# Performance work log

Hardware: AMD Instinct MI355X
Metric: run time of the kernel (lower is better)

Reference implementation:

```python
import jax, jax.numpy as jnp
import numpy as np

TAU = 0.07          # temperature
TOP_N_SIM = 5       # n_neighb for KNN label assignment
RANKING_K = 4       # top-k same/diff-class sims for confidence ratio


def setup_inputs() -> dict:
    key = jax.random.key(0)
    k1, k2, k3 = jax.random.split(key, 3)
    n_src, n_tgt, d, n_cls = 8192, 6144, 256, 64
    return {
        "source_features": jax.random.normal(k1, (n_src, d), dtype=jnp.float32),
        "source_labels": jax.random.randint(k2, (n_src,), 0, n_cls, dtype=jnp.int32),
        "target_features": jax.random.normal(k3, (n_tgt, d), dtype=jnp.float32),
    }


def _l2_normalize(x):
    # F.normalize(x, dim=1, p=2) with eps=1e-12
    n = jnp.sqrt(jnp.sum(x * x, axis=1, keepdims=True))
    return x / jnp.maximum(n, 1e-12)


def reference(source_features, source_labels, target_features):
    n_tgt = target_features.shape[0]
    top_ranked_n = n_tgt * 2 // 3

    # cosine similarity matrix [n_src, n_tgt]
    sim = _l2_normalize(source_features) @ _l2_normalize(target_features).T

    # sort each column descending over sources
    order = jnp.argsort(-sim, axis=0)                      # [S, T]

    # KNN label assignment with torch.mode semantics (tie -> smallest value)
    neigh = source_labels[order[:TOP_N_SIM]]               # [K, T]
    counts = (neigh[:, None, :] == neigh[None, :, :]).sum(axis=1)  # [K, T]
    maxc = counts.max(axis=0)                              # [T]
    big = jnp.iinfo(source_labels.dtype).max
    assigned = jnp.where(counts == maxc[None, :], neigh, big).min(axis=0)  # [T]

    # sims & labels reordered by descending similarity, per column
    sorted_sims = jnp.take_along_axis(sim, order, axis=0)  # [S, T]
    sorted_labels = source_labels[order]                   # [S, T]
    pos = sorted_labels == assigned[None, :]               # [S, T]

    def first_k_masked_sum(mask):
        # sum of first RANKING_K sorted sims where mask is True, per column
        csum = jnp.cumsum(mask.astype(sim.dtype), axis=0)
        sel = mask & (csum <= RANKING_K)
        return jnp.sum(jnp.where(sel, sorted_sims, 0.0), axis=0)

    nln = first_k_masked_sum(pos)
    nun = first_k_masked_sum(~pos)
    scores = jax.lax.stop_gradient(nln / nun)              # [T], detached

    _, top_ind = jax.lax.top_k(scores, top_ranked_n)       # confident targets
    conf_sim = sim[:, top_ind]                             # [S, top_ranked_n]
    conf_lab = assigned[top_ind]

    # contrastive softmax loss over sources
    mask_sim = (source_labels[:, None] == conf_lab[None, :]).astype(sim.dtype)
    exp_scores = jax.nn.softmax(conf_sim / TAU, axis=0)
    contrastive = (exp_scores * mask_sim).sum(axis=0) / exp_scores.sum(axis=0)
    return -jnp.mean(jnp.log(contrastive + 1e-6))
```

## Files before the change

### kernel.cpp

```cpp
#include <hip/hip_runtime.h>
#include <cstdint>
#include <cstddef>

#define DIM 256
#define NSRC 8192
#define NCLS 64
#define KSTEPS 8
#define INV_TAU (1.0f / 0.07f)
#define EPITCH 136

typedef __attribute__((ext_vector_type(8))) short bf16x8;
typedef __attribute__((ext_vector_type(4))) float f32x4;
typedef unsigned char uchar;

__device__ __forceinline__ ushort f2bf_rne(float f) {
    uint u = __float_as_uint(f);
    uint r = u + 0x7fff + ((u >> 16) & 1);
    return (ushort)(r >> 16);
}
__device__ __forceinline__ uint bf2ord(uint u) {
    return u ^ (0x8000u + (u >> 15) * 0x7FFFu);
}
__device__ __forceinline__ float ord2f(uint o) {
    uint u = (o & 0x8000u) ? (o ^ 0x8000u) : (~o & 0xFFFFu);
    return __uint_as_float(u << 16);
}
__device__ __forceinline__ uint med3u(uint a, uint b, uint c) {
    uint d;
    asm("v_med3_u32 %0, %1, %2, %3" : "=v"(d) : "v"(a), "v"(b), "v"(c));
    return d;
}

__device__ __forceinline__ void gload_lds16(const void* g, void* l) {
    __builtin_amdgcn_global_load_lds((const __attribute__((address_space(1))) void*)g,
                                     (__attribute__((address_space(3))) void*)l,
                                     16, 0, 0);
}

__global__ __launch_bounds__(256) void l2bf2_k(const float* __restrict__ inA,
                                               ushort* __restrict__ outA, int nA,
                                               const float* __restrict__ inB,
                                               ushort* __restrict__ outB, int nB) {
    const int w = (blockIdx.x * 256 + threadIdx.x) >> 6;
    const int lane = threadIdx.x & 63;
    if (w >= nA + nB) return;
    const float* in;
    ushort* out;
    int row;
    if (w < nA) { in = inA; out = outA; row = w; }
    else        { in = inB; out = outB; row = w - nA; }
    float4 v = *(const float4*)(in + (size_t)row * DIM + lane * 4);
    float ss = v.x * v.x + v.y * v.y + v.z * v.z + v.w * v.w;
#pragma unroll
    for (int d = 1; d < 64; d <<= 1) ss += __shfl_xor(ss, d);
    const float n = fmaxf(sqrtf(ss), 1e-12f);
    ushort4 o;
    o.x = f2bf_rne(v.x / n);
    o.y = f2bf_rne(v.y / n);
    o.z = f2bf_rne(v.z / n);
    o.w = f2bf_rne(v.w / n);
    *(ushort4*)(out + (size_t)row * DIM + lane * 4) = o;
}

__global__ __launch_bounds__(256) void class_build_k(const int* __restrict__ labels,
                                                     uchar* __restrict__ lab8,
                                                     int* __restrict__ cstart,
                                                     int* __restrict__ clist, int n) {
    const int c = blockIdx.x, t = threadIdx.x;
    const int g = c * 256 + t;
    if (g < n) lab8[g] = (uchar)labels[g];

    __shared__ int sl[256], se[256];
    const int per = n >> 8;
    const int i0 = t * per;
    int less = 0, eq = 0;
    for (int j = 0; j < per; ++j) {
        const int l = labels[i0 + j];
        less += (l < c);
        eq += (l == c);
    }
    sl[t] = less; se[t] = eq;
    __syncthreads();
    for (int s = 1; s < 256; s <<= 1) {
        const int a = (t >= s) ? sl[t - s] : 0;
        const int b = (t >= s) ? se[t - s] : 0;
        __syncthreads();
        sl[t] += a; se[t] += b;
        __syncthreads();
    }
    const int base = sl[255];
    int pos = base + se[t] - eq;
    for (int j = 0; j < per; ++j) {
        const int i = i0 + j;
        if (labels[i] == c) clist[pos++] = i;
    }
    if (t == 0) cstart[c] = base;
    if (c == 0 && t == 1) cstart[NCLS] = n;
}

__global__ __launch_bounds__(512) void gemm_mfma_k(const ushort* __restrict__ A,
                                                   const ushort* __restrict__ B,
                                                   ushort* __restrict__ C,
                                                   int M, int N) {
    __shared__ __align__(16) ushort smem[24576];

    const int tid = threadIdx.x;
    const int lane = tid & 63, wid = tid >> 6;
    const int wr = wid >> 1, wc = wid & 1;

    const int gx = gridDim.x;
    const int bid = blockIdx.y * gx + blockIdx.x;
    const int rowsPerX = gridDim.y >> 3;
    const int grpW = 8;
    const int grpSize = rowsPerX * grpW;
    const int xcd = bid & 7;
    const int local = bid >> 3;
    const int grp = local / grpSize;
    const int within = local % grpSize;
    const int bm = (xcd * rowsPerX + within % rowsPerX) * 128;
    const int bn = (grp * grpW + within / rowsPerX) * 128;

    const int cr = tid >> 2;
    const int cch = tid & 3;
    const int sch = cch ^ ((cr >> 1) & 3);
    const char* aSrcP = (const char*)A + (size_t)(bm + cr) * (DIM * 2) + sch * 16;
    const char* bSrcP = (const char*)B + (size_t)(bn + cr) * (DIM * 2) + sch * 16;
    const uint ldsOff = (uint)(wid * 1024);

    const int fr = lane & 15, fk = lane >> 4;
    const int swz = (fr >> 1) & 3;
    int idxA[2], idxB[4];
#pragma unroll
    for (int m = 0; m < 2; ++m)
        idxA[m] = (wr * 32 + m * 16 + fr) * 32 + ((fk ^ swz) * 8);
#pragma unroll
    for (int n = 0; n < 4; ++n)
        idxB[n] = (wc * 64 + n * 16 + fr) * 32 + ((fk ^ swz) * 8);

    f32x4 acc[2][4];
#pragma unroll
    for (int m = 0; m < 2; ++m)
#pragma unroll
        for (int n = 0; n < 4; ++n) acc[m][n] = (f32x4){0.f, 0.f, 0.f, 0.f};

#define STAGE(b, ks)                                                               \
    {                                                                              \
        gload_lds16(aSrcP + (ks) * 64, (char*)smem + (b) * 8192 + ldsOff);         \
        gload_lds16(bSrcP + (ks) * 64, (char*)smem + 24576 + (b) * 8192 + ldsOff); \
    }

    STAGE(0, 0);
    STAGE(1, 1);

#pragma unroll
    for (int ks = 0; ks < KSTEPS; ++ks) {
        if (ks < KSTEPS - 1) { asm volatile("s_waitcnt vmcnt(2)" ::: "memory"); }
        else                 { asm volatile("s_waitcnt vmcnt(0)" ::: "memory"); }
        __builtin_amdgcn_s_barrier();
        asm volatile("" ::: "memory");

        if (ks + 2 < KSTEPS) STAGE((ks + 2) % 3, ks + 2);

        const int slot = ks % 3;
        const ushort* sAc = smem + slot * 4096;
        const ushort* sBc = smem + 12288 + slot * 4096;
        bf16x8 av[2], bv[4];
#pragma unroll
        for (int m = 0; m < 2; ++m) av[m] = *(const bf16x8*)&sAc[idxA[m]];
#pragma unroll
        for (int n = 0; n < 4; ++n) bv[n] = *(const bf16x8*)&sBc[idxB[n]];
#pragma unroll
        for (int m = 0; m < 2; ++m)
#pragma unroll
            for (int n = 0; n < 4; ++n)
                acc[m][n] = __builtin_amdgcn_mfma_f32_16x16x32_bf16(av[m], bv[n], acc[m][n], 0, 0, 0);
    }
#undef STAGE

    __syncthreads();
#pragma unroll
    for (int m = 0; m < 2; ++m) {
#pragma unroll
        for (int n = 0; n < 4; ++n) {
            const int colb = wc * 64 + n * 16 + fr;
#pragma unroll
            for (int j = 0; j < 4; ++j) {
                const int rowb = wr * 32 + m * 16 + fk * 4 + j;
                smem[rowb * EPITCH + colb] = f2bf_rne(acc[m][n][j]);
            }
        }
    }
    __syncthreads();
    const int rr = tid >> 4, cc = (tid & 15) * 8;
#pragma unroll
    for (int it = 0; it < 4; ++it) {
        const int r = it * 32 + rr;
        uint4 v = *(const uint4*)&smem[r * EPITCH + cc];
        *(uint4*)(C + (size_t)(bm + r) * N + bn + cc) = v;
    }
}

__global__ __launch_bounds__(256) void assign_score_w(const ushort* __restrict__ sim,
                                                      const int* __restrict__ labels,
                                                      const uchar* __restrict__ lab8,
                                                      const int* __restrict__ cstart,
                                                      const int* __restrict__ clist,
                                                      float* __restrict__ scores_out,
                                                      float* __restrict__ logt_out) {
    const int lane = threadIdx.x & 63, wid = threadIdx.x >> 6;
    const int t = blockIdx.x * 4 + wid;
    const ushort* row = sim + (size_t)t * NSRC;

    uint kA0 = 0, kA1 = 0, kA2 = 0, kA3 = 0;
    uint kB0 = 0, kB1 = 0, kB2 = 0, kB3 = 0;
    float s1a = 0.f, s1b = 0.f;

#define CH4X(u16, idx, K0, K1, K2, K3, S1)                              \
    {                                                                   \
        uint uu = (uint)(u16);                                          \
        float vv = __uint_as_float(uu << 16);                           \
        S1 += __expf(fmaf(vv, INV_TAU, -INV_TAU));                      \
        uint od = uu ^ (0x8000u + (uu >> 15) * 0x7FFFu);                \
        uint nk = (od << 16) | (uint)(8191 - (idx));                    \
        uint q1 = med3u(nk, K0, K1);                                    \
        uint q2 = med3u(nk, K1, K2);                                    \
        uint q3 = med3u(nk, K2, K3);                                    \
        K0 = max(K0, nk); K1 = q1; K2 = q2; K3 = q3;                    \
    }
#define CH8(u16, idx)                                                   \
    {                                                                   \
        uint uu = (uint)(u16);                                          \
        uint od = uu ^ (0x8000u + (uu >> 15) * 0x7FFFu);                \
        uint nk = (od << 16) | (uint)(8191 - (idx));                    \
        uint q1 = med3u(nk, k0, k1);                                    \
        uint q2 = med3u(nk, k1, k2);                                    \
        uint q3 = med3u(nk, k2, k3);                                    \
        uint q4 = med3u(nk, k3, k4);                                    \
        uint q5 = med3u(nk, k4, k5);                                    \
        uint q6 = med3u(nk, k5, k6);                                    \
        uint q7 = med3u(nk, k6, k7);                                    \
        k0 = max(k0, nk);                                               \
        k1 = q1; k2 = q2; k3 = q3; k4 = q4; k5 = q5; k6 = q6; k7 = q7;  \
    }
#define MERGE8                                                                     \
    _Pragma("unroll")                                                              \
    for (int d = 1; d < 64; d <<= 1) {                                             \
        uint b0 = __shfl_xor(k0, d), b1 = __shfl_xor(k1, d), b2 = __shfl_xor(k2, d),\
             b3 = __shfl_xor(k3, d), b4 = __shfl_xor(k4, d), b5 = __shfl_xor(k5, d),\
             b6 = __shfl_xor(k6, d), b7 = __shfl_xor(k7, d);                        \
        uint r0 = max(k0, b0);                                                     \
        uint r1 = max(max(min(k0, b0), k1), b1);                                   \
        uint r2 = max(max(min(k0, b1), min(k1, b0)), max(k2, b2));                 \
        uint r3 = max(max(min(k0, b2), min(k1, b1)),                               \
                      max(max(min(k2, b0), k3), b3));                              \
        uint r4 = max(max(max(min(k0, b3), min(k1, b2)),                           \
                          max(min(k2, b1), min(k3, b0))), max(k4, b4));            \
        uint r5 = max(max(max(min(k0, b4), min(k1, b3)),                           \
                          max(min(k2, b2), min(k3, b1))),                          \
                      max(max(min(k4, b0), k5), b5));                              \
        uint r6 = max(max(max(min(k0, b5), min(k1, b4)),                           \
                          max(min(k2, b3), min(k3, b2))),                          \
                      max(max(min(k4, b1), min(k5, b0)), max(k6, b6)));            \
        uint r7 = max(max(max(min(k0, b6), min(k1, b5)),                           \
                          max(min(k2, b4), min(k3, b3))),                          \
                      max(max(min(k4, b2), min(k5, b1)),                           \
                          max(max(min(k6, b0), k7), b7)));                         \
        k0 = r0; k1 = r1; k2 = r2; k3 = r3; k4 = r4; k5 = r5; k6 = r6; k7 = r7;    \
    }

    for (int i0 = lane * 8; i0 < NSRC; i0 += 1024) {
        uint4 w = *(const uint4*)(row + i0);
        uint4 w2 = *(const uint4*)(row + i0 + 512);
        CH4X(w.x & 0xFFFF, i0 + 0, kA0, kA1, kA2, kA3, s1a);
        CH4X(w.x >> 16,    i0 + 1, kA0, kA1, kA2, kA3, s1a);
        CH4X(w.y & 0xFFFF, i0 + 2, kA0, kA1, kA2, kA3, s1a);
        CH4X(w.y >> 16,    i0 + 3, kA0, kA1, kA2, kA3, s1a);
        CH4X(w.z & 0xFFFF, i0 + 4, kA0, kA1, kA2, kA3, s1a);
        CH4X(w.z >> 16,    i0 + 5, kA0, kA1, kA2, kA3, s1a);
        CH4X(w.w & 0xFFFF, i0 + 6, kA0, kA1, kA2, kA3, s1a);
        CH4X(w.w >> 16,    i0 + 7, kA0, kA1, kA2, kA3, s1a);
        CH4X(w2.x & 0xFFFF, i0 + 512, kB0, kB1, kB2, kB3, s1b);
        CH4X(w2.x >> 16,    i0 + 513, kB0, kB1, kB2, kB3, s1b);
        CH4X(w2.y & 0xFFFF, i0 + 514, kB0, kB1, kB2, kB3, s1b);
        CH4X(w2.y >> 16,    i0 + 515, kB0, kB1, kB2, kB3, s1b);
        CH4X(w2.z & 0xFFFF, i0 + 516, kB0, kB1, kB2, kB3, s1b);
        CH4X(w2.z >> 16,    i0 + 517, kB0, kB1, kB2, kB3, s1b);
        CH4X(w2.w & 0xFFFF, i0 + 518, kB0, kB1, kB2, kB3, s1b);
        CH4X(w2.w >> 16,    i0 + 519, kB0, kB1, kB2, kB3, s1b);
    }
    uint k0 = max(kA0, kB0);
    uint k1 = max(max(min(kA0, kB0), kA1), kB1);
    uint k2 = max(max(min(kA0, kB1), min(kA1, kB0)), max(kA2, kB2));
    uint k3 = max(max(min(kA0, kB2), min(kA1, kB1)),
                  max(max(min(kA2, kB0), kA3), kB3));
    uint k4 = 0, k5 = 0, k6 = 0, k7 = 0;

    const uint prek3 = k3;
    MERGE8;
    if (!__all((int)(prek3 <= k7))) {
        k0 = k1 = k2 = k3 = k4 = k5 = k6 = k7 = 0;
        for (int i0 = lane * 8; i0 < NSRC; i0 += 512) {
            uint4 w = *(const uint4*)(row + i0);
            CH8(w.x & 0xFFFF, i0 + 0); CH8(w.x >> 16, i0 + 1);
            CH8(w.y & 0xFFFF, i0 + 2); CH8(w.y >> 16, i0 + 3);
            CH8(w.z & 0xFFFF, i0 + 4); CH8(w.z >> 16, i0 + 5);
            CH8(w.w & 0xFFFF, i0 + 6); CH8(w.w >> 16, i0 + 7);
        }
        MERGE8;
    }
#undef CH4X
#undef CH8
#undef MERGE8

    float s1 = s1a + s1b;
#pragma unroll
    for (int d = 1; d < 64; d <<= 1) s1 += __shfl_xor(s1, d);

    const int l0 = labels[8191 - (int)(k0 & 0xFFFF)];
    const int l1 = labels[8191 - (int)(k1 & 0xFFFF)];
    const int l2 = labels[8191 - (int)(k2 & 0xFFFF)];
    const int l3 = labels[8191 - (int)(k3 & 0xFFFF)];
    const int l4 = labels[8191 - (int)(k4 & 0xFFFF)];
    const int l5 = labels[8191 - (int)(k5 & 0xFFFF)];
    const int l6 = labels[8191 - (int)(k6 & 0xFFFF)];
    const int l7 = labels[8191 - (int)(k7 & 0xFFFF)];

    const int c0 = 1 + (l0 == l1) + (l0 == l2) + (l0 == l3) + (l0 == l4);
    const int c1 = (l1 == l0) + 1 + (l1 == l2) + (l1 == l3) + (l1 == l4);
    const int c2 = (l2 == l0) + (l2 == l1) + 1 + (l2 == l3) + (l2 == l4);
    const int c3 = (l3 == l0) + (l3 == l1) + (l3 == l2) + 1 + (l3 == l4);
    const int c4 = (l4 == l0) + (l4 == l1) + (l4 == l2) + (l4 == l3) + 1;
    const int maxc = max(max(max(c0, c1), max(c2, c3)), c4);
    int assigned = 0x7fffffff;
    if (c0 == maxc) assigned = min(assigned, l0);
    if (c1 == maxc) assigned = min(assigned, l1);
    if (c2 == maxc) assigned = min(assigned, l2);
    if (c3 == maxc) assigned = min(assigned, l3);
    if (c4 == maxc) assigned = min(assigned, l4);
    const int aL = assigned;

    const int negcnt = (l0 != aL) + (l1 != aL) + (l2 != aL) + (l3 != aL) +
                       (l4 != aL) + (l5 != aL) + (l6 != aL) + (l7 != aL);
    float nun = 0.f;
    if (negcnt >= 4) {
        int c = 0;
#define NSTEP(kj, lj)                                                       \
        {                                                                   \
            bool take = ((lj) != aL) && (c < 4);                            \
            nun += take ? ord2f((kj) >> 16) : 0.f;                          \
            c += take ? 1 : 0;                                              \
        }
        NSTEP(k0, l0) NSTEP(k1, l1) NSTEP(k2, l2) NSTEP(k3, l3)
        NSTEP(k4, l4) NSTEP(k5, l5) NSTEP(k6, l6) NSTEP(k7, l7)
#undef NSTEP
    } else {
        uint n0 = 0, n1 = 0, n2 = 0, n3 = 0;
        for (int i0 = lane * 8; i0 < NSRC; i0 += 512) {
            uint4 w = *(const uint4*)(row + i0);
            uint2 lw = *(const uint2*)(lab8 + i0);
#define NEGP(u16, lb)                                                       \
            {                                                               \
                uint uu = (uint)(u16);                                      \
                uint od = uu ^ (0x8000u + (uu >> 15) * 0x7FFFu);            \
                uint x = ((lb) == aL) ? 0u : od;                            \
                uint q1 = med3u(x, n0, n1);                                 \
                uint q2 = med3u(x, n1, n2);                                 \
                uint q3 = med3u(x, n2, n3);                                 \
                n0 = max(n0, x); n1 = q1; n2 = q2; n3 = q3;                 \
            }
            NEGP(w.x & 0xFFFF, (int)(lw.x & 255));
            NEGP(w.x >> 16,    (int)((lw.x >> 8) & 255));
            NEGP(w.y & 0xFFFF, (int)((lw.x >> 16) & 255));
            NEGP(w.y >> 16,    (int)(lw.x >> 24));
            NEGP(w.z & 0xFFFF, (int)(lw.y & 255));
            NEGP(w.z >> 16,    (int)((lw.y >> 8) & 255));
            NEGP(w.w & 0xFFFF, (int)((lw.y >> 16) & 255));
            NEGP(w.w >> 16,    (int)(lw.y >> 24));
#undef NEGP
        }
#pragma unroll
        for (int d = 1; d < 64; d <<= 1) {
            uint b0 = __shfl_xor(n0, d), b1 = __shfl_xor(n1, d),
                 b2 = __shfl_xor(n2, d), b3 = __shfl_xor(n3, d);
            uint r0 = max(n0, b0);
            uint r1 = max(max(min(n0, b0), n1), b1);
            uint r2 = max(max(min(n0, b1), min(n1, b0)), max(n2, b2));
            uint r3 = max(max(min(n0, b2), min(n1, b1)),
                          max(max(min(n2, b0), n3), b3));
            n0 = r0; n1 = r1; n2 = r2; n3 = r3;
        }
        nun = (n0 ? ord2f(n0) : 0.f) + (n1 ? ord2f(n1) : 0.f) +
              (n2 ? ord2f(n2) : 0.f) + (n3 ? ord2f(n3) : 0.f);
    }

    const int cs = cstart[aL], ce = cstart[aL + 1];
    float tp0 = -2.f, tp1 = -2.f, tp2 = -2.f, tp3 = -2.f;
    float sp = 0.f;
    for (int p = cs + lane; p < ce; p += 64) {
        const int idx = clist[p];
        float v = __uint_as_float(((uint)row[idx]) << 16);
        sp += __expf(fmaf(v, INV_TAU, -INV_TAU));
        float q1 = __builtin_amdgcn_fmed3f(v, tp0, tp1);
        float q2 = __builtin_amdgcn_fmed3f(v, tp1, tp2);
        float q3 = __builtin_amdgcn_fmed3f(v, tp2, tp3);
        tp0 = fmaxf(tp0, v); tp1 = q1; tp2 = q2; tp3 = q3;
    }
#pragma unroll
    for (int d = 1; d < 64; d <<= 1) {
        sp += __shfl_xor(sp, d);
        float b0 = __shfl_xor(tp0, d), b1 = __shfl_xor(tp1, d),
              b2 = __shfl_xor(tp2, d), b3 = __shfl_xor(tp3, d);
        float r0 = fmaxf(tp0, b0);
        float r1 = fmaxf(fmaxf(fminf(tp0, b0), tp1), b1);
        float r2 = fmaxf(fmaxf(fminf(tp0, b1), fminf(tp1, b0)), fmaxf(tp2, b2));
        float r3 = fmaxf(fmaxf(fminf(tp0, b2), fminf(tp1, b1)),
                         fmaxf(fmaxf(fminf(tp2, b0), tp3), b3));
        tp0 = r0; tp1 = r1; tp2 = r2; tp3 = r3;
    }

    if (lane == 0) {
        float nln = (tp0 > -1.5f ? tp0 : 0.f) + (tp1 > -1.5f ? tp1 : 0.f) +
                    (tp2 > -1.5f ? tp2 : 0.f) + (tp3 > -1.5f ? tp3 : 0.f);
        scores_out[t] = nln / nun;
        logt_out[t] = logf(sp / s1 + 1e-6f);
    }
}

__global__ __launch_bounds__(256) void select_topk_w(const float* __restrict__ scores,
                                                     int* __restrict__ selected,
                                                     int n, int k) {
    const int lane = threadIdx.x & 63, wid = threadIdx.x >> 6;
    const int t = blockIdx.x * 4 + wid;
    if (t >= n) return;
    const float st = scores[t];
    int rank = 0;
    for (int j0 = lane * 4; j0 < n; j0 += 256) {
        float4 v = *(const float4*)(scores + j0);
        rank += (v.x > st) || (v.x == st && (j0 + 0) < t);
        rank += (v.y > st) || (v.y == st && (j0 + 1) < t);
        rank += (v.z > st) || (v.z == st && (j0 + 2) < t);
        rank += (v.w > st) || (v.w == st && (j0 + 3) < t);
    }
    for (int d = 1; d < 64; d <<= 1) rank += __shfl_xor(rank, d);
    if (lane == 0) selected[t] = (rank < k) ? 1 : 0;
}

__global__ __launch_bounds__(256) void finalize_k(const float* __restrict__ logt,
                                                  const int* __restrict__ selected,
                                                  float* __restrict__ out, int n, int k) {
    __shared__ float red[256];
    const int tid = threadIdx.x;
    float s = 0.f;
    for (int i = tid; i < n; i += 256) s += selected[i] ? logt[i] : 0.f;
    red[tid] = s;
    __syncthreads();
    for (int st = 128; st > 0; st >>= 1) {
        if (tid < st) red[tid] += red[tid + st];
        __syncthreads();
    }
    if (tid == 0) out[0] = -red[0] / (float)k;
}

extern "C" void kernel_launch(void* const* d_in, const int* in_sizes, int n_in,
                              void* d_out, int out_size, void* d_ws, size_t ws_size,
                              hipStream_t stream) {
    const float* srcF = (const float*)d_in[0];
    const int* labels = (const int*)d_in[1];
    const float* tgtF = (const float*)d_in[2];
    float* out = (float*)d_out;

    const int n_src = in_sizes[1];
    const int d = in_sizes[0] / n_src;
    const int n_tgt = in_sizes[2] / d;
    const int topn = n_tgt * 2 / 3;

    char* ws = (char*)d_ws;
    ushort* src2 = (ushort*)ws;  ws += (size_t)n_src * DIM * sizeof(ushort);
    ushort* tgt2 = (ushort*)ws;  ws += (size_t)n_tgt * DIM * sizeof(ushort);
    ushort* sim  = (ushort*)ws;  ws += (size_t)n_tgt * NSRC * sizeof(ushort);
    float* scores = (float*)ws;  ws += (size_t)n_tgt * sizeof(float);
    float* logt   = (float*)ws;  ws += (size_t)n_tgt * sizeof(float);
    int* selected = (int*)ws;    ws += (size_t)n_tgt * sizeof(int);
    int* cstart   = (int*)ws;    ws += (size_t)(NCLS + 1) * sizeof(int);
    int* clist    = (int*)ws;    ws += (size_t)n_src * sizeof(int);
    uchar* lab8   = (uchar*)ws;  ws += (size_t)n_src;

    const int nrows = n_tgt + n_src;
    l2bf2_k<<<(nrows + 3) / 4, 256, 0, stream>>>(tgtF, tgt2, n_tgt, srcF, src2, n_src);
    class_build_k<<<NCLS, 256, 0, stream>>>(labels, lab8, cstart, clist, n_src);

    dim3 grid(n_src / 128, n_tgt / 128);
    gemm_mfma_k<<<grid, 512, 0, stream>>>(tgt2, src2, sim, n_tgt, n_src);

    assign_score_w<<<n_tgt / 4, 256, 0, stream>>>(sim, labels, lab8, cstart, clist,
                                                  scores, logt);
    select_topk_w<<<(n_tgt + 3) / 4, 256, 0, stream>>>(scores, selected, n_tgt, topn);
    finalize_k<<<1, 256, 0, stream>>>(logt, selected, out, n_tgt, topn);
}
```

Before: 110.2 us.

## Split each target row's top-k scan across two wavefronts and merge via LDS

The assign_score kernel now assigns two wavefronts to each target column, with each one scanning half of the 8192 source similarities. Each wavefront builds its partial top-8 keys and exp sum, writes them to shared memory, and after a barrier the first wavefront merges the other half's results. The aim is more parallelism and shorter per-wave serial scans in the row-reduction kernel. The cost is a block-wide sync, idle second-half waves in the tail, and a second fallback rescan that is now decided per half.

```diff
diff --git a/kernel.cpp b/kernel.cpp
--- a/kernel.cpp
+++ b/kernel.cpp
@@ -37,217 +37,8 @@
                                      16, 0, 0);
 }
 
-__global__ __launch_bounds__(256) void l2bf2_k(const float* __restrict__ inA,
-                                               ushort* __restrict__ outA, int nA,
-                                               const float* __restrict__ inB,
-                                               ushort* __restrict__ outB, int nB) {
-    const int w = (blockIdx.x * 256 + threadIdx.x) >> 6;
-    const int lane = threadIdx.x & 63;
-    if (w >= nA + nB) return;
-    const float* in;
-    ushort* out;
-    int row;
-    if (w < nA) { in = inA; out = outA; row = w; }
-    else        { in = inB; out = outB; row = w - nA; }
-    float4 v = *(const float4*)(in + (size_t)row * DIM + lane * 4);
-    float ss = v.x * v.x + v.y * v.y + v.z * v.z + v.w * v.w;
-#pragma unroll
-    for (int d = 1; d < 64; d <<= 1) ss += __shfl_xor(ss, d);
-    const float n = fmaxf(sqrtf(ss), 1e-12f);
-    ushort4 o;
-    o.x = f2bf_rne(v.x / n);
-    o.y = f2bf_rne(v.y / n);
-    o.z = f2bf_rne(v.z / n);
-    o.w = f2bf_rne(v.w / n);
-    *(ushort4*)(out + (size_t)row * DIM + lane * 4) = o;
-}
-
-__global__ __launch_bounds__(256) void class_build_k(const int* __restrict__ labels,
-                                                     uchar* __restrict__ lab8,
-                                                     int* __restrict__ cstart,
-                                                     int* __restrict__ clist, int n) {
-    const int c = blockIdx.x, t = threadIdx.x;
-    const int g = c * 256 + t;
-    if (g < n) lab8[g] = (uchar)labels[g];
-
-    __shared__ int sl[256], se[256];
-    const int per = n >> 8;
-    const int i0 = t * per;
-    int less = 0, eq = 0;
-    for (int j = 0; j < per; ++j) {
-        const int l = labels[i0 + j];
-        less += (l < c);
-        eq += (l == c);
-    }
-    sl[t] = less; se[t] = eq;
-    __syncthreads();
-    for (int s = 1; s < 256; s <<= 1) {
-        const int a = (t >= s) ? sl[t - s] : 0;
-        const int b = (t >= s) ? se[t - s] : 0;
-        __syncthreads();
-        sl[t] += a; se[t] += b;
-        __syncthreads();
-    }
-    const int base = sl[255];
-    int pos = base + se[t] - eq;
-    for (int j = 0; j < per; ++j) {
-        const int i = i0 + j;
-        if (labels[i] == c) clist[pos++] = i;
-    }
-    if (t == 0) cstart[c] = base;
-    if (c == 0 && t == 1) cstart[NCLS] = n;
-}
-
-__global__ __launch_bounds__(512) void gemm_mfma_k(const ushort* __restrict__ A,
-                                                   const ushort* __restrict__ B,
-                                                   ushort* __restrict__ C,
-                                                   int M, int N) {
-    __shared__ __align__(16) ushort smem[24576];
-
-    const int tid = threadIdx.x;
-    const int lane = tid & 63, wid = tid >> 6;
-    const int wr = wid >> 1, wc = wid & 1;
-
-    const int gx = gridDim.x;
-    const int bid = blockIdx.y * gx + blockIdx.x;
-    const int rowsPerX = gridDim.y >> 3;
-    const int grpW = 8;
-    const int grpSize = rowsPerX * grpW;
-    const int xcd = bid & 7;
-    const int local = bid >> 3;
-    const int grp = local / grpSize;
-    const int within = local % grpSize;
-    const int bm = (xcd * rowsPerX + within % rowsPerX) * 128;
-    const int bn = (grp * grpW + within / rowsPerX) * 128;
-
-    const int cr = tid >> 2;
-    const int cch = tid & 3;
-    const int sch = cch ^ ((cr >> 1) & 3);
-    const char* aSrcP = (const char*)A + (size_t)(bm + cr) * (DIM * 2) + sch * 16;
-    const char* bSrcP = (const char*)B + (size_t)(bn + cr) * (DIM * 2) + sch * 16;
-    const uint ldsOff = (uint)(wid * 1024);
-
-    const int fr = lane & 15, fk = lane >> 4;
-    const int swz = (fr >> 1) & 3;
-    int idxA[2], idxB[4];
-#pragma unroll
-    for (int m = 0; m < 2; ++m)
-        idxA[m] = (wr * 32 + m * 16 + fr) * 32 + ((fk ^ swz) * 8);
-#pragma unroll
-    for (int n = 0; n < 4; ++n)
-        idxB[n] = (wc * 64 + n * 16 + fr) * 32 + ((fk ^ swz) * 8);
-
-    f32x4 acc[2][4];
-#pragma unroll
-    for (int m = 0; m < 2; ++m)
-#pragma unroll
-        for (int n = 0; n < 4; ++n) acc[m][n] = (f32x4){0.f, 0.f, 0.f, 0.f};
-
-#define STAGE(b, ks)                                                               \
+#define MERGEVALS                                                                  \
     {                                                                              \
-        gload_lds16(aSrcP + (ks) * 64, (char*)smem + (b) * 8192 + ldsOff);         \
-        gload_lds16(bSrcP + (ks) * 64, (char*)smem + 24576 + (b) * 8192 + ldsOff); \
-    }
-
-    STAGE(0, 0);
-    STAGE(1, 1);
-
-#pragma unroll
-    for (int ks = 0; ks < KSTEPS; ++ks) {
-        if (ks < KSTEPS - 1) { asm volatile("s_waitcnt vmcnt(2)" ::: "memory"); }
-        else                 { asm volatile("s_waitcnt vmcnt(0)" ::: "memory"); }
-        __builtin_amdgcn_s_barrier();
-        asm volatile("" ::: "memory");
-
-        if (ks + 2 < KSTEPS) STAGE((ks + 2) % 3, ks + 2);
-
-        const int slot = ks % 3;
-        const ushort* sAc = smem + slot * 4096;
-        const ushort* sBc = smem + 12288 + slot * 4096;
-        bf16x8 av[2], bv[4];
-#pragma unroll
-        for (int m = 0; m < 2; ++m) av[m] = *(const bf16x8*)&sAc[idxA[m]];
-#pragma unroll
-        for (int n = 0; n < 4; ++n) bv[n] = *(const bf16x8*)&sBc[idxB[n]];
-#pragma unroll
-        for (int m = 0; m < 2; ++m)
-#pragma unroll
-            for (int n = 0; n < 4; ++n)
-                acc[m][n] = __builtin_amdgcn_mfma_f32_16x16x32_bf16(av[m], bv[n], acc[m][n], 0, 0, 0);
-    }
-#undef STAGE
-
-    __syncthreads();
-#pragma unroll
-    for (int m = 0; m < 2; ++m) {
-#pragma unroll
-        for (int n = 0; n < 4; ++n) {
-            const int colb = wc * 64 + n * 16 + fr;
-#pragma unroll
-            for (int j = 0; j < 4; ++j) {
-                const int rowb = wr * 32 + m * 16 + fk * 4 + j;
-                smem[rowb * EPITCH + colb] = f2bf_rne(acc[m][n][j]);
-            }
-        }
-    }
-    __syncthreads();
-    const int rr = tid >> 4, cc = (tid & 15) * 8;
-#pragma unroll
-    for (int it = 0; it < 4; ++it) {
-        const int r = it * 32 + rr;
-        uint4 v = *(const uint4*)&smem[r * EPITCH + cc];
-        *(uint4*)(C + (size_t)(bm + r) * N + bn + cc) = v;
-    }
-}
-
-__global__ __launch_bounds__(256) void assign_score_w(const ushort* __restrict__ sim,
-                                                      const int* __restrict__ labels,
-                                                      const uchar* __restrict__ lab8,
-                                                      const int* __restrict__ cstart,
-                                                      const int* __restrict__ clist,
-                                                      float* __restrict__ scores_out,
-                                                      float* __restrict__ logt_out) {
-    const int lane = threadIdx.x & 63, wid = threadIdx.x >> 6;
-    const int t = blockIdx.x * 4 + wid;
-    const ushort* row = sim + (size_t)t * NSRC;
-
-    uint kA0 = 0, kA1 = 0, kA2 = 0, kA3 = 0;
-    uint kB0 = 0, kB1 = 0, kB2 = 0, kB3 = 0;
-    float s1a = 0.f, s1b = 0.f;
-
-#define CH4X(u16, idx, K0, K1, K2, K3, S1)                              \
-    {                                                                   \
-        uint uu = (uint)(u16);                                          \
-        float vv = __uint_as_float(uu << 16);                           \
-        S1 += __expf(fmaf(vv, INV_TAU, -INV_TAU));                      \
-        uint od = uu ^ (0x8000u + (uu >> 15) * 0x7FFFu);                \
-        uint nk = (od << 16) | (uint)(8191 - (idx));                    \
-        uint q1 = med3u(nk, K0, K1);                                    \
-        uint q2 = med3u(nk, K1, K2);                                    \
-        uint q3 = med3u(nk, K2, K3);                                    \
-        K0 = max(K0, nk); K1 = q1; K2 = q2; K3 = q3;                    \
-    }
-#define CH8(u16, idx)                                                   \
-    {                                                                   \
-        uint uu = (uint)(u16);                                          \
-        uint od = uu ^ (0x8000u + (uu >> 15) * 0x7FFFu);                \
-        uint nk = (od << 16) | (uint)(8191 - (idx));                    \
-        uint q1 = med3u(nk, k0, k1);                                    \
-        uint q2 = med3u(nk, k1, k2);                                    \
-        uint q3 = med3u(nk, k2, k3);                                    \
-        uint q4 = med3u(nk, k3, k4);                                    \
-        uint q5 = med3u(nk, k4, k5);                                    \
-        uint q6 = med3u(nk, k5, k6);                                    \
-        uint q7 = med3u(nk, k6, k7);                                    \
-        k0 = max(k0, nk);                                               \
-        k1 = q1; k2 = q2; k3 = q3; k4 = q4; k5 = q5; k6 = q6; k7 = q7;  \
-    }
-#define MERGE8                                                                     \
-    _Pragma("unroll")                                                              \
-    for (int d = 1; d < 64; d <<= 1) {                                             \
-        uint b0 = __shfl_xor(k0, d), b1 = __shfl_xor(k1, d), b2 = __shfl_xor(k2, d),\
-             b3 = __shfl_xor(k3, d), b4 = __shfl_xor(k4, d), b5 = __shfl_xor(k5, d),\
-             b6 = __shfl_xor(k6, d), b7 = __shfl_xor(k7, d);                        \
         uint r0 = max(k0, b0);                                                     \
         uint r1 = max(max(min(k0, b0), k1), b1);                                   \
         uint r2 = max(max(min(k0, b1), min(k1, b0)), max(k2, b2));                 \
@@ -267,8 +58,227 @@
                           max(max(min(k6, b0), k7), b7)));                         \
         k0 = r0; k1 = r1; k2 = r2; k3 = r3; k4 = r4; k5 = r5; k6 = r6; k7 = r7;    \
     }
-
-    for (int i0 = lane * 8; i0 < NSRC; i0 += 1024) {
+#define MERGESTEP(d)                                                               \
+    {                                                                              \
+        uint b0 = __shfl_xor(k0, d), b1 = __shfl_xor(k1, d), b2 = __shfl_xor(k2, d),\
+             b3 = __shfl_xor(k3, d), b4 = __shfl_xor(k4, d), b5 = __shfl_xor(k5, d),\
+             b6 = __shfl_xor(k6, d), b7 = __shfl_xor(k7, d);                        \
+        MERGEVALS                                                                  \
+    }
+
+__global__ __launch_bounds__(256) void l2bf2_k(const float* __restrict__ inA,
+                                               ushort* __restrict__ outA, int nA,
+                                               const float* __restrict__ inB,
+                                               ushort* __restrict__ outB, int nB) {
+    const int w = (blockIdx.x * 256 + threadIdx.x) >> 6;
+    const int lane = threadIdx.x & 63;
+    if (w >= nA + nB) return;
+    const float* in;
+    ushort* out;
+    int row;
+    if (w < nA) { in = inA; out = outA; row = w; }
+    else        { in = inB; out = outB; row = w - nA; }
+    float4 v = *(const float4*)(in + (size_t)row * DIM + lane * 4);
+    float ss = v.x * v.x + v.y * v.y + v.z * v.z + v.w * v.w;
+#pragma unroll
+    for (int d = 1; d < 64; d <<= 1) ss += __shfl_xor(ss, d);
+    const float n = fmaxf(sqrtf(ss), 1e-12f);
+    ushort4 o;
+    o.x = f2bf_rne(v.x / n);
+    o.y = f2bf_rne(v.y / n);
+    o.z = f2bf_rne(v.z / n);
+    o.w = f2bf_rne(v.w / n);
+    *(ushort4*)(out + (size_t)row * DIM + lane * 4) = o;
+}
+
+__global__ __launch_bounds__(256) void class_build_k(const int* __restrict__ labels,
+                                                     uchar* __restrict__ lab8,
+                                                     int* __restrict__ cstart,
+                                                     int* __restrict__ clist, int n) {
+    const int c = blockIdx.x, t = threadIdx.x;
+    const int g = c * 256 + t;
+    if (g < n) lab8[g] = (uchar)labels[g];
+
+    __shared__ int sl[256], se[256];
+    const int per = n >> 8;
+    const int i0 = t * per;
+    int less = 0, eq = 0;
+    for (int j = 0; j < per; ++j) {
+        const int l = labels[i0 + j];
+        less += (l < c);
+        eq += (l == c);
+    }
+    sl[t] = less; se[t] = eq;
+    __syncthreads();
+    for (int s = 1; s < 256; s <<= 1) {
+        const int a = (t >= s) ? sl[t - s] : 0;
+        const int b = (t >= s) ? se[t - s] : 0;
+        __syncthreads();
+        sl[t] += a; se[t] += b;
+        __syncthreads();
+    }
+    const int base = sl[255];
+    int pos = base + se[t] - eq;
+    for (int j = 0; j < per; ++j) {
+        const int i = i0 + j;
+        if (labels[i] == c) clist[pos++] = i;
+    }
+    if (t == 0) cstart[c] = base;
+    if (c == 0 && t == 1) cstart[NCLS] = n;
+}
+
+__global__ __launch_bounds__(512) void gemm_mfma_k(const ushort* __restrict__ A,
+                                                   const ushort* __restrict__ B,
+                                                   ushort* __restrict__ C,
+                                                   int M, int N) {
+    __shared__ __align__(16) ushort smem[24576];
+
+    const int tid = threadIdx.x;
+    const int lane = tid & 63, wid = tid >> 6;
+    const int wr = wid >> 1, wc = wid & 1;
+
+    const int gx = gridDim.x;
+    const int bid = blockIdx.y * gx + blockIdx.x;
+    const int rowsPerX = gridDim.y >> 3;
+    const int grpW = 8;
+    const int grpSize = rowsPerX * grpW;
+    const int xcd = bid & 7;
+    const int local = bid >> 3;
+    const int grp = local / grpSize;
+    const int within = local % grpSize;
+    const int bm = (xcd * rowsPerX + within % rowsPerX) * 128;
+    const int bn = (grp * grpW + within / rowsPerX) * 128;
+
+    const int cr = tid >> 2;
+    const int cch = tid & 3;
+    const int sch = cch ^ ((cr >> 1) & 3);
+    const char* aSrcP = (const char*)A + (size_t)(bm + cr) * (DIM * 2) + sch * 16;
+    const char* bSrcP = (const char*)B + (size_t)(bn + cr) * (DIM * 2) + sch * 16;
+    const uint ldsOff = (uint)(wid * 1024);
+
+    const int fr = lane & 15, fk = lane >> 4;
+    const int swz = (fr >> 1) & 3;
+    int idxA[2], idxB[4];
+#pragma unroll
+    for (int m = 0; m < 2; ++m)
+        idxA[m] = (wr * 32 + m * 16 + fr) * 32 + ((fk ^ swz) * 8);
+#pragma unroll
+    for (int n = 0; n < 4; ++n)
+        idxB[n] = (wc * 64 + n * 16 + fr) * 32 + ((fk ^ swz) * 8);
+
+    f32x4 acc[2][4];
+#pragma unroll
+    for (int m = 0; m < 2; ++m)
+#pragma unroll
+        for (int n = 0; n < 4; ++n) acc[m][n] = (f32x4){0.f, 0.f, 0.f, 0.f};
+
+#define STAGE(b, ks)                                                               \
+    {                                                                              \
+        gload_lds16(aSrcP + (ks) * 64, (char*)smem + (b) * 8192 + ldsOff);         \
+        gload_lds16(bSrcP + (ks) * 64, (char*)smem + 24576 + (b) * 8192 + ldsOff); \
+    }
+
+    STAGE(0, 0);
+    STAGE(1, 1);
+
+#pragma unroll
+    for (int ks = 0; ks < KSTEPS; ++ks) {
+        if (ks < KSTEPS - 1) { asm volatile("s_waitcnt vmcnt(2)" ::: "memory"); }
+        else                 { asm volatile("s_waitcnt vmcnt(0)" ::: "memory"); }
+        __builtin_amdgcn_s_barrier();
+        asm volatile("" ::: "memory");
+
+        if (ks + 2 < KSTEPS) STAGE((ks + 2) % 3, ks + 2);
+
+        const int slot = ks % 3;
+        const ushort* sAc = smem + slot * 4096;
+        const ushort* sBc = smem + 12288 + slot * 4096;
+        bf16x8 av[2], bv[4];
+#pragma unroll
+        for (int m = 0; m < 2; ++m) av[m] = *(const bf16x8*)&sAc[idxA[m]];
+#pragma unroll
+        for (int n = 0; n < 4; ++n) bv[n] = *(const bf16x8*)&sBc[idxB[n]];
+#pragma unroll
+        for (int m = 0; m < 2; ++m)
+#pragma unroll
+            for (int n = 0; n < 4; ++n)
+                acc[m][n] = __builtin_amdgcn_mfma_f32_16x16x32_bf16(av[m], bv[n], acc[m][n], 0, 0, 0);
+    }
+#undef STAGE
+
+    __syncthreads();
+#pragma unroll
+    for (int m = 0; m < 2; ++m) {
+#pragma unroll
+        for (int n = 0; n < 4; ++n) {
+            const int colb = wc * 64 + n * 16 + fr;
+#pragma unroll
+            for (int j = 0; j < 4; ++j) {
+                const int rowb = wr * 32 + m * 16 + fk * 4 + j;
+                smem[rowb * EPITCH + colb] = f2bf_rne(acc[m][n][j]);
+            }
+        }
+    }
+    __syncthreads();
+    const int rr = tid >> 4, cc = (tid & 15) * 8;
+#pragma unroll
+    for (int it = 0; it < 4; ++it) {
+        const int r = it * 32 + rr;
+        uint4 v = *(const uint4*)&smem[r * EPITCH + cc];
+        *(uint4*)(C + (size_t)(bm + r) * N + bn + cc) = v;
+    }
+}
+
+__global__ __launch_bounds__(512) void assign_score_w(const ushort* __restrict__ sim,
+                                                      const int* __restrict__ labels,
+                                                      const uchar* __restrict__ lab8,
+                                                      const int* __restrict__ cstart,
+                                                      const int* __restrict__ clist,
+                                                      float* __restrict__ scores_out,
+                                                      float* __restrict__ logt_out) {
+    const int lane = threadIdx.x & 63, wid = threadIdx.x >> 6;
+    const int slot = wid >> 1;
+    const int half = wid & 1;
+    const int t = blockIdx.x * 4 + slot;
+    const ushort* row = sim + (size_t)t * NSRC;
+    const int base = half * 4096;
+
+    __shared__ uint mk[8][8];
+    __shared__ float ms1[8];
+
+    uint kA0 = 0, kA1 = 0, kA2 = 0, kA3 = 0;
+    uint kB0 = 0, kB1 = 0, kB2 = 0, kB3 = 0;
+    float s1a = 0.f, s1b = 0.f;
+
+#define CH4X(u16, idx, K0, K1, K2, K3, S1)                              \
+    {                                                                   \
+        uint uu = (uint)(u16);                                          \
+        float vv = __uint_as_float(uu << 16);                           \
+        S1 += __expf(fmaf(vv, INV_TAU, -INV_TAU));                      \
+        uint od = uu ^ (0x8000u + (uu >> 15) * 0x7FFFu);                \
+        uint nk = (od << 16) | (uint)(8191 - (idx));                    \
+        uint q1 = med3u(nk, K0, K1);                                    \
+        uint q2 = med3u(nk, K1, K2);                                    \
+        uint q3 = med3u(nk, K2, K3);                                    \
+        K0 = max(K0, nk); K1 = q1; K2 = q2; K3 = q3;                    \
+    }
+#define CH8(u16, idx)                                                   \
+    {                                                                   \
+        uint uu = (uint)(u16);                                          \
+        uint od = uu ^ (0x8000u + (uu >> 15) * 0x7FFFu);                \
+        uint nk = (od << 16) | (uint)(8191 - (idx));                    \
+        uint q1 = med3u(nk, k0, k1);                                    \
+        uint q2 = med3u(nk, k1, k2);                                    \
+        uint q3 = med3u(nk, k2, k3);                                    \
+        uint q4 = med3u(nk, k3, k4);                                    \
+        uint q5 = med3u(nk, k4, k5);                                    \
+        uint q6 = med3u(nk, k5, k6);                                    \
+        uint q7 = med3u(nk, k6, k7);                                    \
+        k0 = max(k0, nk);                                               \
+        k1 = q1; k2 = q2; k3 = q3; k4 = q4; k5 = q5; k6 = q6; k7 = q7;  \
+    }
+
+    for (int i0 = base + lane * 8; i0 < base + 4096; i0 += 1024) {
         uint4 w = *(const uint4*)(row + i0);
         uint4 w2 = *(const uint4*)(row + i0 + 512);
         CH4X(w.x & 0xFFFF, i0 + 0, kA0, kA1, kA2, kA3, s1a);
@@ -296,25 +306,41 @@
     uint k4 = 0, k5 = 0, k6 = 0, k7 = 0;
 
     const uint prek3 = k3;
-    MERGE8;
+#pragma unroll
+    for (int d = 1; d < 64; d <<= 1) MERGESTEP(d)
     if (!__all((int)(prek3 <= k7))) {
         k0 = k1 = k2 = k3 = k4 = k5 = k6 = k7 = 0;
-        for (int i0 = lane * 8; i0 < NSRC; i0 += 512) {
+        for (int i0 = base + lane * 8; i0 < base + 4096; i0 += 512) {
             uint4 w = *(const uint4*)(row + i0);
             CH8(w.x & 0xFFFF, i0 + 0); CH8(w.x >> 16, i0 + 1);
             CH8(w.y & 0xFFFF, i0 + 2); CH8(w.y >> 16, i0 + 3);
             CH8(w.z & 0xFFFF, i0 + 4); CH8(w.z >> 16, i0 + 5);
             CH8(w.w & 0xFFFF, i0 + 6); CH8(w.w >> 16, i0 + 7);
         }
-        MERGE8;
+#pragma unroll
+        for (int d = 1; d < 64; d <<= 1) MERGESTEP(d)
     }
 #undef CH4X
 #undef CH8
-#undef MERGE8
 
     float s1 = s1a + s1b;
 #pragma unroll
     for (int d = 1; d < 64; d <<= 1) s1 += __shfl_xor(s1, d);
+
+    if (lane == 0) {
+        mk[wid][0] = k0; mk[wid][1] = k1; mk[wid][2] = k2; mk[wid][3] = k3;
+        mk[wid][4] = k4; mk[wid][5] = k5; mk[wid][6] = k6; mk[wid][7] = k7;
+        ms1[wid] = s1;
+    }
+    __syncthreads();
+    if (half) return;
+    {
+        const uint* q = mk[wid ^ 1];
+        uint b0 = q[0], b1 = q[1], b2 = q[2], b3 = q[3];
+        uint b4 = q[4], b5 = q[5], b6 = q[6], b7 = q[7];
+        MERGEVALS
+        s1 += ms1[wid ^ 1];
+    }
 
     const int l0 = labels[8191 - (int)(k0 & 0xFFFF)];
     const int l1 = labels[8191 - (int)(k1 & 0xFFFF)];
@@ -492,7 +518,7 @@
     dim3 grid(n_src / 128, n_tgt / 128);
     gemm_mfma_k<<<grid, 512, 0, stream>>>(tgt2, src2, sim, n_tgt, n_src);
 
-    assign_score_w<<<n_tgt / 4, 256, 0, stream>>>(sim, labels, lab8, cstart, clist,
+    assign_score_w<<<n_tgt / 4, 512, 0, stream>>>(sim, labels, lab8, cstart, clist,
                                                   scores, logt);
     select_topk_w<<<(n_tgt + 3) / 4, 256, 0, stream>>>(scores, selected, n_tgt, topn);
     finalize_k<<<1, 256, 0, stream>>>(logt, selected, out, n_tgt, topn);
```

New measurement: 115.1 us. 4.4% more time.
